# Kernel optimization log

Measured on AMD Instinct MI355X. Metric: run time of the kernel, lower is better.

## Reference

```python
import jax, jax.numpy as jnp
import numpy as np

HEAD_DIM = 64

def setup_inputs() -> dict:
    key = jax.random.key(0)
    k1, k2, k3 = jax.random.split(key, 3)
    B, L, D = 2, 2048, 1024
    x = jax.random.normal(k1, (B, L, D), dtype=jnp.float32)
    # torch nn.Linear weights are [out_features, in_features]
    w_qkv = jax.random.normal(k2, (3 * D, D), dtype=jnp.float32) * (D ** -0.5)
    w_out = jax.random.normal(k3, (D, D), dtype=jnp.float32) * (D ** -0.5)
    # causal mask: True = attend (masked_fill on logical_not)
    mask = jnp.tril(jnp.ones((L, L), dtype=bool))[None].repeat(B, axis=0)
    return {"x": x, "mask": mask, "w_qkv": w_qkv, "w_out": w_out}

def reference(x, mask, w_qkv, w_out):
    B, L, D = x.shape
    H, Hd = D // HEAD_DIM, HEAD_DIM
    scale = Hd ** -0.5
    qkv = x @ w_qkv.T                               # [B, L, 3D]
    q, k, v = jnp.split(qkv, 3, axis=-1)
    # [B, L, D] -> [B, H, L, Hd]
    def split_heads(t):
        return t.reshape(B, L, H, Hd).transpose(0, 2, 1, 3)
    q, k, v = split_heads(q), split_heads(k), split_heads(v)
    attn = jnp.einsum('bhld,bhmd->bhlm', q, k) * scale  # [B, H, L, L]
    attn = jnp.where(mask[:, None, :, :], attn, -jnp.inf)
    attn = jax.nn.softmax(attn, axis=-1)
    out = jnp.einsum('bhlm,bhmd->bhld', attn, v)        # [B, H, L, Hd]
    out = out.transpose(0, 2, 1, 3).reshape(B, L, D)
    return out @ w_out.T
```

## Files before the change

### kernel.cpp

```cpp
#include <hip/hip_runtime.h>
#include <hip/hip_bf16.h>


typedef __bf16 bf16;
typedef __bf16 bf16x8 __attribute__((ext_vector_type(8)));
typedef __bf16 bf16x4 __attribute__((ext_vector_type(4)));
typedef float  f32x4  __attribute__((ext_vector_type(4)));

#define MFMA16(a, b, c) __builtin_amdgcn_mfma_f32_16x16x32_bf16(a, b, c, 0, 0, 0)

__global__ __launch_bounds__(256) void cvt_all(
    const float* __restrict__ x, const float* __restrict__ wq,
    const float* __restrict__ wo, bf16* __restrict__ dst) {
  int i = blockIdx.x * 256 + threadIdx.x;
  const float* src;
  int off;
  if (i < 1048576) {
    src = x; off = i;
  } else if (i < 1048576 + 786432) {
    src = wq; off = i - 1048576;
  } else {
    src = wo; off = i - (1048576 + 786432);
  }
  float4 v = ((const float4*)src)[off];
  bf16x4 o;
  o[0] = (bf16)v.x; o[1] = (bf16)v.y; o[2] = (bf16)v.z; o[3] = (bf16)v.w;
  ((bf16x4*)dst)[i] = o;
}

__device__ __forceinline__ void gload_lds16(const bf16* g, bf16* l) {
  __builtin_amdgcn_global_load_lds(
      (const __attribute__((address_space(1))) void*)g,
      (__attribute__((address_space(3))) void*)l, 16, 0, 0);
}

template <int ROWS>
__device__ __forceinline__ void stage_tile(const bf16* __restrict__ src, int ld,
                                           bf16* lds, int tid) {
  const int wid = tid >> 6;
#pragma unroll
  for (int i = 0; i < ROWS / 32; ++i) {
    int c = i * 256 + tid;
    int row = c >> 3;
    int slot = (c & 7) ^ (row & 7);
    gload_lds16(src + row * ld + slot * 8, lds + i * 2048 + wid * 512);
  }
}

__device__ __forceinline__ bf16x8 read_swz(const bf16* lds, int row, int kbyte) {
  int byte = row * 128 + (kbyte ^ ((row & 7) << 4));
  return *(const bf16x8*)((const char*)lds + byte);
}

template <int MODE>
__global__ __launch_bounds__(256) void gemm_nt(
    const bf16* __restrict__ A, const bf16* __restrict__ Bt,
    bf16* __restrict__ C0, bf16* __restrict__ C1, bf16* __restrict__ C2,
    float* __restrict__ Cf,
    int M, int N, int K, int nbm) {
  __shared__ bf16 ldsA[128 * 64];
  __shared__ bf16 ldsB[128 * 64];
  const int tid = threadIdx.x;
  const int lane = tid & 63, wid = tid >> 6;
  const int wr = wid >> 1, wc = wid & 1;
  const int bm = blockIdx.x % nbm, bn = blockIdx.x / nbm;
  const int l15 = lane & 15, g = lane >> 4;

  f32x4 acc[4][4] = {};
  const bf16* Ab = A + (size_t)bm * 128 * K;
  const bf16* Bb = Bt + (size_t)bn * 128 * K;

  for (int k0 = 0; k0 < K; k0 += 64) {
    __syncthreads();
    stage_tile<128>(Ab + k0, K, ldsA, tid);
    stage_tile<128>(Bb + k0, K, ldsB, tid);
    __syncthreads();
#pragma unroll
    for (int kc = 0; kc < 2; ++kc) {
      bf16x8 af[4], bfr[4];
#pragma unroll
      for (int mi = 0; mi < 4; ++mi)
        af[mi] = read_swz(ldsA, wr * 64 + mi * 16 + l15, kc * 64 + g * 16);
#pragma unroll
      for (int ni = 0; ni < 4; ++ni)
        bfr[ni] = read_swz(ldsB, wc * 64 + ni * 16 + l15, kc * 64 + g * 16);
#pragma unroll
      for (int mi = 0; mi < 4; ++mi)
#pragma unroll
        for (int ni = 0; ni < 4; ++ni)
          acc[mi][ni] = MFMA16(af[mi], bfr[ni], acc[mi][ni]);
    }
  }

  const int mbase = bm * 128 + wr * 64, nbase = bn * 128 + wc * 64;
#pragma unroll
  for (int mi = 0; mi < 4; ++mi) {
#pragma unroll
    for (int ni = 0; ni < 4; ++ni) {
#pragma unroll
      for (int r = 0; r < 4; ++r) {
        int m = mbase + mi * 16 + g * 4 + r;
        int n = nbase + ni * 16 + l15;
        if (MODE == 0) {
          Cf[(size_t)m * N + n] = acc[mi][ni][r];
        } else {
          bf16 v = (bf16)acc[mi][ni][r];
          int part = n >> 10;
          int hh = (n >> 6) & 15, hd = n & 63;
          int bb = m >> 11, ll = m & 2047;
          size_t bhb = (size_t)(bb * 16 + hh);
          if (part == 2) {
            C2[(bhb * 64 + hd) * 2048 + ll] = v;
          } else {
            bf16* dst = (part == 0) ? C0 : C1;
            dst[(bhb * 2048 + ll) * 64 + hd] = v;
          }
        }
      }
    }
  }
}

__global__ __launch_bounds__(256) void attn_fwd(
    const bf16* __restrict__ Q, const bf16* __restrict__ Kb,
    const bf16* __restrict__ Vt, bf16* __restrict__ O2) {
  __shared__ bf16 ldsK[2][64 * 64];
  __shared__ bf16 ldsVt[2][64 * 64];
  __shared__ bf16 ldsP[4][16 * 64];

  const int tid = threadIdx.x, lane = tid & 63, wid = tid >> 6;
  const int l15 = lane & 15, g = lane >> 4;
  const int qt = 31 - (blockIdx.x >> 5);
  const int bh = blockIdx.x & 31;
  const int b = bh >> 4, h = bh & 15;
  const bf16* Qh  = Q  + (size_t)bh * 2048 * 64;
  const bf16* Kh  = Kb + (size_t)bh * 2048 * 64;
  const bf16* VtH = Vt + (size_t)bh * 64 * 2048;
  const int q0 = qt * 64;
  const int qrow = q0 + wid * 16 + l15;

  const float CE = 0.18033688011112042f;

  bf16x8 qf[2];
#pragma unroll
  for (int dk = 0; dk < 2; ++dk)
    qf[dk] = *(const bf16x8*)(Qh + (size_t)qrow * 64 + dk * 32 + g * 8);

  float m_run = -__builtin_inff();
  float l_lane = 0.f;
  f32x4 oacc[4] = {};

  auto step = [&](bool masked, int curb) {
    f32x4 s[4] = {};
#pragma unroll
    for (int sub = 0; sub < 4; ++sub) {
#pragma unroll
      for (int dk = 0; dk < 2; ++dk) {
        bf16x8 kf = read_swz(&ldsK[curb][0], sub * 16 + l15, dk * 64 + g * 16);
        s[sub] = MFMA16(kf, qf[dk], s[sub]);
      }
    }
    if (masked) {
#pragma unroll
      for (int sub = 0; sub < 4; ++sub)
#pragma unroll
        for (int r = 0; r < 4; ++r) {
          int kvl = sub * 16 + g * 4 + r;
          if (kvl > wid * 16 + l15) s[sub][r] = -__builtin_inff();
        }
    }
    float m0 = fmaxf(fmaxf(s[0][0], s[0][1]), fmaxf(s[0][2], s[0][3]));
    float m1 = fmaxf(fmaxf(s[1][0], s[1][1]), fmaxf(s[1][2], s[1][3]));
    float m2 = fmaxf(fmaxf(s[2][0], s[2][1]), fmaxf(s[2][2], s[2][3]));
    float m3 = fmaxf(fmaxf(s[3][0], s[3][1]), fmaxf(s[3][2], s[3][3]));
    float mt = fmaxf(fmaxf(m0, m1), fmaxf(m2, m3));
    mt = fmaxf(mt, __shfl_xor(mt, 16));
    mt = fmaxf(mt, __shfl_xor(mt, 32));
    if (!__all(mt <= m_run)) {
      float mnew = fmaxf(m_run, mt);
      float alpha = exp2f((m_run - mnew) * CE);
#pragma unroll
      for (int dsub = 0; dsub < 4; ++dsub) {
        oacc[dsub][0] *= alpha; oacc[dsub][1] *= alpha;
        oacc[dsub][2] *= alpha; oacc[dsub][3] *= alpha;
      }
      l_lane *= alpha;
      m_run = mnew;
    }
    float lsum = 0.f;
#pragma unroll
    for (int sub = 0; sub < 4; ++sub) {
      bf16x4 pb;
#pragma unroll
      for (int r = 0; r < 4; ++r) {
        float e = exp2f((s[sub][r] - m_run) * CE);
        lsum += e;
        pb[r] = (bf16)e;
      }
      int kbyte = sub * 32 + g * 8;
      *(bf16x4*)((char*)&ldsP[wid][0] +
                 (l15 * 128 + (kbyte ^ ((l15 & 7) << 4)))) = pb;
    }
    l_lane += lsum;
#pragma unroll
    for (int kc = 0; kc < 2; ++kc) {
      bf16x8 pf = read_swz(&ldsP[wid][0], l15, kc * 64 + g * 16);
#pragma unroll
      for (int dsub = 0; dsub < 4; ++dsub) {
        bf16x8 vf = read_swz(&ldsVt[curb][0], dsub * 16 + l15, kc * 64 + g * 16);
        oacc[dsub] = MFMA16(vf, pf, oacc[dsub]);
      }
    }
  };

  stage_tile<64>(Kh, 64, &ldsK[0][0], tid);
  stage_tile<64>(VtH, 2048, &ldsVt[0][0], tid);
  __syncthreads();

  int cur = 0;
  for (int t = 0; t < qt; ++t) {
    stage_tile<64>(Kh + (size_t)(t + 1) * 64 * 64, 64, &ldsK[cur ^ 1][0], tid);
    stage_tile<64>(VtH + (t + 1) * 64, 2048, &ldsVt[cur ^ 1][0], tid);
    step(false, cur);
    __syncthreads();
    cur ^= 1;
  }
  step(true, cur);

  float l_run = l_lane;
  l_run += __shfl_xor(l_run, 16);
  l_run += __shfl_xor(l_run, 32);
  const float linv = 1.f / l_run;
#pragma unroll
  for (int dsub = 0; dsub < 4; ++dsub)
#pragma unroll
    for (int r = 0; r < 4; ++r) {
      int d = dsub * 16 + g * 4 + r;
      O2[((size_t)(b * 2048 + qrow)) * 1024 + h * 64 + d] =
          (bf16)(oacc[dsub][r] * linv);
    }
}

extern "C" void kernel_launch(void* const* d_in, const int* in_sizes, int n_in,
                              void* d_out, int out_size, void* d_ws, size_t ws_size,
                              hipStream_t stream) {
  const float* x     = (const float*)d_in[0];
  const float* w_qkv = (const float*)d_in[2];
  const float* w_out = (const float*)d_in[3];
  float* out = (float*)d_out;

  char* ws = (char*)d_ws;
  bf16* xb    = (bf16*)(ws);
  bf16* wqkvb = (bf16*)(ws + ((size_t)8 << 20));
  bf16* woutb = (bf16*)(ws + ((size_t)14 << 20));
  bf16* Qb    = (bf16*)(ws + ((size_t)16 << 20));
  bf16* Kbuf  = (bf16*)(ws + ((size_t)24 << 20));
  bf16* Vtb   = (bf16*)(ws + ((size_t)32 << 20));
  bf16* O2    = (bf16*)(ws + ((size_t)40 << 20));

  cvt_all<<<dim3(8192), 256, 0, stream>>>(x, w_qkv, w_out, xb);

  gemm_nt<1><<<dim3(32 * 24), 256, 0, stream>>>(xb, wqkvb, Qb, Kbuf, Vtb,
                                                nullptr, 4096, 3072, 1024, 32);
  attn_fwd<<<dim3(32 * 32), 256, 0, stream>>>(Qb, Kbuf, Vtb, O2);
  gemm_nt<0><<<dim3(32 * 8), 256, 0, stream>>>(O2, woutb, nullptr, nullptr,
                                               nullptr, out, 4096, 1024, 1024, 32);
}
```

Before: 199.1 us.

## Share K/V tiles across two query tiles with 8-wave attention blocks

The attention kernel now launches 512-thread blocks that each handle two adjacent 64-row query tiles, so every K/Vt tile staged into LDS serves twice as many query rows. This roughly halves global K/V traffic and the number of blocks. Alongside this, the swizzled LDS offsets are precomputed, the exp path switches to __expf with the 0.125 scale folded into an fma, and the cross-lane max shuffle runs only when a rescale is needed. In exchange, the lower half of each block sits idle on its last tile, and the larger blocks may lower occupancy.

```diff
diff --git a/kernel.cpp b/kernel.cpp
--- a/kernel.cpp
+++ b/kernel.cpp
@@ -45,6 +45,13 @@
     int slot = (c & 7) ^ (row & 7);
     gload_lds16(src + row * ld + slot * 8, lds + i * 2048 + wid * 512);
   }
+}
+
+__device__ __forceinline__ void stage_tile512(const bf16* __restrict__ src,
+                                              int ld, bf16* lds, int tid) {
+  int row = tid >> 3;
+  int slot = (tid & 7) ^ (row & 7);
+  gload_lds16(src + row * ld + slot * 8, lds + (tid >> 6) * 512);
 }
 
 __device__ __forceinline__ bf16x8 read_swz(const bf16* lds, int row, int kbyte) {
@@ -121,25 +128,40 @@
   }
 }
 
-__global__ __launch_bounds__(256) void attn_fwd(
+__global__ __launch_bounds__(512) void attn_fwd8(
     const bf16* __restrict__ Q, const bf16* __restrict__ Kb,
     const bf16* __restrict__ Vt, bf16* __restrict__ O2) {
   __shared__ bf16 ldsK[2][64 * 64];
   __shared__ bf16 ldsVt[2][64 * 64];
-  __shared__ bf16 ldsP[4][16 * 64];
+  __shared__ bf16 ldsP[8 * 1024];
 
   const int tid = threadIdx.x, lane = tid & 63, wid = tid >> 6;
   const int l15 = lane & 15, g = lane >> 4;
-  const int qt = 31 - (blockIdx.x >> 5);
+  const int wsub = wid & 3;
+  const int half = wid >> 2;
+  const int qpair = 15 - (blockIdx.x >> 5);
   const int bh = blockIdx.x & 31;
   const int b = bh >> 4, h = bh & 15;
   const bf16* Qh  = Q  + (size_t)bh * 2048 * 64;
   const bf16* Kh  = Kb + (size_t)bh * 2048 * 64;
   const bf16* VtH = Vt + (size_t)bh * 64 * 2048;
-  const int q0 = qt * 64;
-  const int qrow = q0 + wid * 16 + l15;
-
-  const float CE = 0.18033688011112042f;
+  const int qbase = qpair * 128;
+  const int qrow = qbase + half * 64 + wsub * 16 + l15;
+  const int myqt = 2 * qpair + half;
+  const int nt = 2 * qpair + 2;
+
+  int off_rd[4][2];
+#pragma unroll
+  for (int r4 = 0; r4 < 4; ++r4)
+#pragma unroll
+    for (int dk = 0; dk < 2; ++dk)
+      off_rd[r4][dk] = (r4 * 16 + l15) * 128 +
+                       ((dk * 64 + g * 16) ^ ((l15 & 7) << 4));
+  int off_pw[4];
+#pragma unroll
+  for (int s4 = 0; s4 < 4; ++s4)
+    off_pw[s4] = l15 * 128 + ((s4 * 32 + g * 8) ^ ((l15 & 7) << 4));
+  char* Pw = (char*)&ldsP[wid * 1024];
 
   bf16x8 qf[2];
 #pragma unroll
@@ -150,13 +172,13 @@
   float l_lane = 0.f;
   f32x4 oacc[4] = {};
 
-  auto step = [&](bool masked, int curb) {
+  auto step = [&](bool masked, const char* Kt, const char* Vtt) {
     f32x4 s[4] = {};
 #pragma unroll
     for (int sub = 0; sub < 4; ++sub) {
 #pragma unroll
       for (int dk = 0; dk < 2; ++dk) {
-        bf16x8 kf = read_swz(&ldsK[curb][0], sub * 16 + l15, dk * 64 + g * 16);
+        bf16x8 kf = *(const bf16x8*)(Kt + off_rd[sub][dk]);
         s[sub] = MFMA16(kf, qf[dk], s[sub]);
       }
     }
@@ -166,19 +188,21 @@
 #pragma unroll
         for (int r = 0; r < 4; ++r) {
           int kvl = sub * 16 + g * 4 + r;
-          if (kvl > wid * 16 + l15) s[sub][r] = -__builtin_inff();
+          if (kvl > wsub * 16 + l15) s[sub][r] = -__builtin_inff();
         }
     }
-    float m0 = fmaxf(fmaxf(s[0][0], s[0][1]), fmaxf(s[0][2], s[0][3]));
-    float m1 = fmaxf(fmaxf(s[1][0], s[1][1]), fmaxf(s[1][2], s[1][3]));
-    float m2 = fmaxf(fmaxf(s[2][0], s[2][1]), fmaxf(s[2][2], s[2][3]));
-    float m3 = fmaxf(fmaxf(s[3][0], s[3][1]), fmaxf(s[3][2], s[3][3]));
-    float mt = fmaxf(fmaxf(m0, m1), fmaxf(m2, m3));
-    mt = fmaxf(mt, __shfl_xor(mt, 16));
-    mt = fmaxf(mt, __shfl_xor(mt, 32));
-    if (!__all(mt <= m_run)) {
+    float a0 = fmaxf(fmaxf(s[0][0], s[0][1]), s[0][2]);
+    float a1 = fmaxf(fmaxf(s[0][3], s[1][0]), s[1][1]);
+    float a2 = fmaxf(fmaxf(s[1][2], s[1][3]), s[2][0]);
+    float a3 = fmaxf(fmaxf(s[2][1], s[2][2]), s[2][3]);
+    float a4 = fmaxf(fmaxf(s[3][0], s[3][1]), s[3][2]);
+    float lmax = fmaxf(fmaxf(fmaxf(a0, a1), fmaxf(a2, a3)),
+                       fmaxf(a4, s[3][3]));
+    if (!__all(lmax <= m_run)) {
+      float mt = fmaxf(lmax, __shfl_xor(lmax, 16));
+      mt = fmaxf(mt, __shfl_xor(mt, 32));
       float mnew = fmaxf(m_run, mt);
-      float alpha = exp2f((m_run - mnew) * CE);
+      float alpha = __expf(0.125f * (m_run - mnew));
 #pragma unroll
       for (int dsub = 0; dsub < 4; ++dsub) {
         oacc[dsub][0] *= alpha; oacc[dsub][1] *= alpha;
@@ -187,45 +211,46 @@
       l_lane *= alpha;
       m_run = mnew;
     }
-    float lsum = 0.f;
+    const float nms = -0.125f * m_run;
+    float ls[4];
 #pragma unroll
     for (int sub = 0; sub < 4; ++sub) {
       bf16x4 pb;
-#pragma unroll
-      for (int r = 0; r < 4; ++r) {
-        float e = exp2f((s[sub][r] - m_run) * CE);
-        lsum += e;
-        pb[r] = (bf16)e;
-      }
-      int kbyte = sub * 32 + g * 8;
-      *(bf16x4*)((char*)&ldsP[wid][0] +
-                 (l15 * 128 + (kbyte ^ ((l15 & 7) << 4)))) = pb;
-    }
-    l_lane += lsum;
+      float e0 = __expf(__builtin_fmaf(s[sub][0], 0.125f, nms));
+      float e1 = __expf(__builtin_fmaf(s[sub][1], 0.125f, nms));
+      float e2 = __expf(__builtin_fmaf(s[sub][2], 0.125f, nms));
+      float e3 = __expf(__builtin_fmaf(s[sub][3], 0.125f, nms));
+      pb[0] = (bf16)e0; pb[1] = (bf16)e1; pb[2] = (bf16)e2; pb[3] = (bf16)e3;
+      ls[sub] = (e0 + e1) + (e2 + e3);
+      *(bf16x4*)(Pw + off_pw[sub]) = pb;
+    }
+    l_lane += (ls[0] + ls[1]) + (ls[2] + ls[3]);
 #pragma unroll
     for (int kc = 0; kc < 2; ++kc) {
-      bf16x8 pf = read_swz(&ldsP[wid][0], l15, kc * 64 + g * 16);
+      bf16x8 pf = *(const bf16x8*)(Pw + off_rd[0][kc]);
 #pragma unroll
       for (int dsub = 0; dsub < 4; ++dsub) {
-        bf16x8 vf = read_swz(&ldsVt[curb][0], dsub * 16 + l15, kc * 64 + g * 16);
+        bf16x8 vf = *(const bf16x8*)(Vtt + off_rd[dsub][kc]);
         oacc[dsub] = MFMA16(vf, pf, oacc[dsub]);
       }
     }
   };
 
-  stage_tile<64>(Kh, 64, &ldsK[0][0], tid);
-  stage_tile<64>(VtH, 2048, &ldsVt[0][0], tid);
+  stage_tile512(Kh, 64, &ldsK[0][0], tid);
+  stage_tile512(VtH, 2048, &ldsVt[0][0], tid);
   __syncthreads();
 
   int cur = 0;
-  for (int t = 0; t < qt; ++t) {
-    stage_tile<64>(Kh + (size_t)(t + 1) * 64 * 64, 64, &ldsK[cur ^ 1][0], tid);
-    stage_tile<64>(VtH + (t + 1) * 64, 2048, &ldsVt[cur ^ 1][0], tid);
-    step(false, cur);
+  for (int t = 0; t < nt; ++t) {
+    if (t + 1 < nt) {
+      stage_tile512(Kh + (size_t)(t + 1) * 64 * 64, 64, &ldsK[cur ^ 1][0], tid);
+      stage_tile512(VtH + (t + 1) * 64, 2048, &ldsVt[cur ^ 1][0], tid);
+    }
+    if (t <= myqt)
+      step(t == myqt, (const char*)&ldsK[cur][0], (const char*)&ldsVt[cur][0]);
     __syncthreads();
     cur ^= 1;
   }
-  step(true, cur);
 
   float l_run = l_lane;
   l_run += __shfl_xor(l_run, 16);
@@ -262,7 +287,7 @@
 
   gemm_nt<1><<<dim3(32 * 24), 256, 0, stream>>>(xb, wqkvb, Qb, Kbuf, Vtb,
                                                 nullptr, 4096, 3072, 1024, 32);
-  attn_fwd<<<dim3(32 * 32), 256, 0, stream>>>(Qb, Kbuf, Vtb, O2);
+  attn_fwd8<<<dim3(32 * 16), 512, 0, stream>>>(Qb, Kbuf, Vtb, O2);
   gemm_nt<0><<<dim3(32 * 8), 256, 0, stream>>>(O2, woutb, nullptr, nullptr,
                                                nullptr, out, 4096, 1024, 1024, 32);
 }
```

After: 203.2 us. 1.02x slower.

## Load K and V fragments directly from global memory in attention, drop LDS staging

Applied to the files above, without the earlier changes.

The attention kernel no longer double-buffers K and V tiles in shared memory with block-wide barriers. Each wave now reads its K and V MFMA fragments straight from global memory, relying on L1/L2 caching because all four waves read the same tiles. It also replaces exp2f with a scaled __expf computed via fma, precomputes the P-buffer swizzle offsets, and reduces the row max across lanes only when a rescale is needed. Removing the barriers lets waves run independently, at the risk of exposing global-load latency with no overlap and fetching each tile four times.

```diff
diff --git a/kernel.cpp b/kernel.cpp
--- a/kernel.cpp
+++ b/kernel.cpp
@@ -121,25 +121,34 @@
   }
 }
 
-__global__ __launch_bounds__(256) void attn_fwd(
+__global__ __launch_bounds__(256) void attn_direct(
     const bf16* __restrict__ Q, const bf16* __restrict__ Kb,
     const bf16* __restrict__ Vt, bf16* __restrict__ O2) {
-  __shared__ bf16 ldsK[2][64 * 64];
-  __shared__ bf16 ldsVt[2][64 * 64];
   __shared__ bf16 ldsP[4][16 * 64];
 
   const int tid = threadIdx.x, lane = tid & 63, wid = tid >> 6;
   const int l15 = lane & 15, g = lane >> 4;
-  const int qt = 31 - (blockIdx.x >> 5);
-  const int bh = blockIdx.x & 31;
+  const int bid = blockIdx.x;
+  const int qt = 31 - (bid >> 5);
+  const int bh = bid & 31;
   const int b = bh >> 4, h = bh & 15;
   const bf16* Qh  = Q  + (size_t)bh * 2048 * 64;
   const bf16* Kh  = Kb + (size_t)bh * 2048 * 64;
   const bf16* VtH = Vt + (size_t)bh * 64 * 2048;
-  const int q0 = qt * 64;
-  const int qrow = q0 + wid * 16 + l15;
-
-  const float CE = 0.18033688011112042f;
+  const int qrow = qt * 64 + wid * 16 + l15;
+  const int nt = qt + 1;
+
+  const int koff = l15 * 64 + g * 8;
+  const int voff = l15 * 2048 + g * 8;
+
+  int offPw[4], offPr[2];
+#pragma unroll
+  for (int s4 = 0; s4 < 4; ++s4)
+    offPw[s4] = l15 * 128 + ((s4 * 32 + g * 8) ^ ((l15 & 7) << 4));
+#pragma unroll
+  for (int kc = 0; kc < 2; ++kc)
+    offPr[kc] = l15 * 128 + ((kc * 64 + g * 16) ^ ((l15 & 7) << 4));
+  char* Pw = (char*)&ldsP[wid][0];
 
   bf16x8 qf[2];
 #pragma unroll
@@ -150,35 +159,45 @@
   float l_lane = 0.f;
   f32x4 oacc[4] = {};
 
-  auto step = [&](bool masked, int curb) {
-    f32x4 s[4] = {};
+  const bf16* Kp = Kh;
+  const bf16* Vp = VtH;
+
+  for (int t = 0; t < nt; ++t) {
+    const bool diag = (t == nt - 1);
+    bf16x8 kfr[4][2];
+#pragma unroll
+    for (int sub = 0; sub < 4; ++sub)
+#pragma unroll
+      for (int dk = 0; dk < 2; ++dk)
+        kfr[sub][dk] = *(const bf16x8*)(Kp + koff + sub * 1024 + dk * 32);
+    f32x4 sv[4] = {};
 #pragma unroll
     for (int sub = 0; sub < 4; ++sub) {
-#pragma unroll
-      for (int dk = 0; dk < 2; ++dk) {
-        bf16x8 kf = read_swz(&ldsK[curb][0], sub * 16 + l15, dk * 64 + g * 16);
-        s[sub] = MFMA16(kf, qf[dk], s[sub]);
-      }
-    }
-    if (masked) {
+      sv[sub] = MFMA16(kfr[sub][0], qf[0], sv[sub]);
+      sv[sub] = MFMA16(kfr[sub][1], qf[1], sv[sub]);
+    }
+    if (diag) {
+      const int rloc = wid * 16 + l15;
 #pragma unroll
       for (int sub = 0; sub < 4; ++sub)
 #pragma unroll
         for (int r = 0; r < 4; ++r) {
           int kvl = sub * 16 + g * 4 + r;
-          if (kvl > wid * 16 + l15) s[sub][r] = -__builtin_inff();
+          if (kvl > rloc) sv[sub][r] = -__builtin_inff();
         }
     }
-    float m0 = fmaxf(fmaxf(s[0][0], s[0][1]), fmaxf(s[0][2], s[0][3]));
-    float m1 = fmaxf(fmaxf(s[1][0], s[1][1]), fmaxf(s[1][2], s[1][3]));
-    float m2 = fmaxf(fmaxf(s[2][0], s[2][1]), fmaxf(s[2][2], s[2][3]));
-    float m3 = fmaxf(fmaxf(s[3][0], s[3][1]), fmaxf(s[3][2], s[3][3]));
-    float mt = fmaxf(fmaxf(m0, m1), fmaxf(m2, m3));
-    mt = fmaxf(mt, __shfl_xor(mt, 16));
-    mt = fmaxf(mt, __shfl_xor(mt, 32));
-    if (!__all(mt <= m_run)) {
+    float a0 = fmaxf(fmaxf(sv[0][0], sv[0][1]), sv[0][2]);
+    float a1 = fmaxf(fmaxf(sv[0][3], sv[1][0]), sv[1][1]);
+    float a2 = fmaxf(fmaxf(sv[1][2], sv[1][3]), sv[2][0]);
+    float a3 = fmaxf(fmaxf(sv[2][1], sv[2][2]), sv[2][3]);
+    float a4 = fmaxf(fmaxf(sv[3][0], sv[3][1]), sv[3][2]);
+    float lmax = fmaxf(fmaxf(fmaxf(a0, a1), fmaxf(a2, a3)),
+                       fmaxf(a4, sv[3][3]));
+    if (!__all(lmax <= m_run)) {
+      float mt = fmaxf(lmax, __shfl_xor(lmax, 16));
+      mt = fmaxf(mt, __shfl_xor(mt, 32));
       float mnew = fmaxf(m_run, mt);
-      float alpha = exp2f((m_run - mnew) * CE);
+      float alpha = __expf(0.125f * (m_run - mnew));
 #pragma unroll
       for (int dsub = 0; dsub < 4; ++dsub) {
         oacc[dsub][0] *= alpha; oacc[dsub][1] *= alpha;
@@ -187,45 +206,32 @@
       l_lane *= alpha;
       m_run = mnew;
     }
-    float lsum = 0.f;
+    const float nms = -0.125f * m_run;
+    float ls = 0.f;
 #pragma unroll
     for (int sub = 0; sub < 4; ++sub) {
+      float e0 = __expf(__builtin_fmaf(sv[sub][0], 0.125f, nms));
+      float e1 = __expf(__builtin_fmaf(sv[sub][1], 0.125f, nms));
+      float e2 = __expf(__builtin_fmaf(sv[sub][2], 0.125f, nms));
+      float e3 = __expf(__builtin_fmaf(sv[sub][3], 0.125f, nms));
       bf16x4 pb;
-#pragma unroll
-      for (int r = 0; r < 4; ++r) {
-        float e = exp2f((s[sub][r] - m_run) * CE);
-        lsum += e;
-        pb[r] = (bf16)e;
+      pb[0] = (bf16)e0; pb[1] = (bf16)e1; pb[2] = (bf16)e2; pb[3] = (bf16)e3;
+      ls += (e0 + e1) + (e2 + e3);
+      *(bf16x4*)(Pw + offPw[sub]) = pb;
+    }
+    l_lane += ls;
+#pragma unroll
+    for (int kc = 0; kc < 2; ++kc) {
+      bf16x8 pf = *(const bf16x8*)(Pw + offPr[kc]);
+#pragma unroll
+      for (int d4 = 0; d4 < 4; ++d4) {
+        bf16x8 vf = *(const bf16x8*)(Vp + voff + d4 * 32768 + kc * 32);
+        oacc[d4] = MFMA16(vf, pf, oacc[d4]);
       }
-      int kbyte = sub * 32 + g * 8;
-      *(bf16x4*)((char*)&ldsP[wid][0] +
-                 (l15 * 128 + (kbyte ^ ((l15 & 7) << 4)))) = pb;
-    }
-    l_lane += lsum;
-#pragma unroll
-    for (int kc = 0; kc < 2; ++kc) {
-      bf16x8 pf = read_swz(&ldsP[wid][0], l15, kc * 64 + g * 16);
-#pragma unroll
-      for (int dsub = 0; dsub < 4; ++dsub) {
-        bf16x8 vf = read_swz(&ldsVt[curb][0], dsub * 16 + l15, kc * 64 + g * 16);
-        oacc[dsub] = MFMA16(vf, pf, oacc[dsub]);
-      }
-    }
-  };
-
-  stage_tile<64>(Kh, 64, &ldsK[0][0], tid);
-  stage_tile<64>(VtH, 2048, &ldsVt[0][0], tid);
-  __syncthreads();
-
-  int cur = 0;
-  for (int t = 0; t < qt; ++t) {
-    stage_tile<64>(Kh + (size_t)(t + 1) * 64 * 64, 64, &ldsK[cur ^ 1][0], tid);
-    stage_tile<64>(VtH + (t + 1) * 64, 2048, &ldsVt[cur ^ 1][0], tid);
-    step(false, cur);
-    __syncthreads();
-    cur ^= 1;
-  }
-  step(true, cur);
+    }
+    Kp += 4096;
+    Vp += 64;
+  }
 
   float l_run = l_lane;
   l_run += __shfl_xor(l_run, 16);
@@ -262,7 +268,7 @@
 
   gemm_nt<1><<<dim3(32 * 24), 256, 0, stream>>>(xb, wqkvb, Qb, Kbuf, Vtb,
                                                 nullptr, 4096, 3072, 1024, 32);
-  attn_fwd<<<dim3(32 * 32), 256, 0, stream>>>(Qb, Kbuf, Vtb, O2);
+  attn_direct<<<dim3(32 * 32), 256, 0, stream>>>(Qb, Kbuf, Vtb, O2);
   gemm_nt<0><<<dim3(32 * 8), 256, 0, stream>>>(O2, woutb, nullptr, nullptr,
                                                nullptr, out, 4096, 1024, 1024, 32);
 }
```

New measurement: 299.5 us. 1.5x slower.
